# Optimization experiments

Hardware: AMD Instinct MI355X
Metric: run time of the kernel (lower is better)

The kernel has to match this reference:

```python
import jax, jax.numpy as jnp
import numpy as np


def _conv3x3(x, w, b):
    # NCHW conv, stride 1, pad 1
    y = jax.lax.conv_general_dilated(x, w, (1, 1), ((1, 1), (1, 1)),
                                     dimension_numbers=('NCHW', 'OIHW', 'NCHW'))
    return y + b[None, :, None, None]


def _deform_conv3x3(x, offset, w):
    # Deformable conv v1: 3x3, stride 1, pad 1, 1 deformable group, no bias.
    # offset: [B, 18, H, W] laid out as (dy_k, dx_k) for k = 0..8 (row-major taps).
    B, C, H, W = x.shape
    K = 9
    off = offset.reshape(B, K, 2, H, W)
    ky, kx = jnp.meshgrid(jnp.arange(3), jnp.arange(3), indexing='ij')
    ky = (ky.reshape(K) - 1).astype(x.dtype)  # kernel tap y-offset, pad=1
    kx = (kx.reshape(K) - 1).astype(x.dtype)
    hh = jnp.arange(H, dtype=x.dtype)
    ww = jnp.arange(W, dtype=x.dtype)
    # sampling locations [B, K, H, W]
    sy = hh[None, None, :, None] + ky[None, :, None, None] + off[:, :, 0]
    sx = ww[None, None, None, :] + kx[None, :, None, None] + off[:, :, 1]
    y0 = jnp.floor(sy)
    x0 = jnp.floor(sx)
    ly = sy - y0  # fractional parts
    lx = sx - x0
    x_flat = x.reshape(B, C, H * W)

    def gather(yi, xi, wgt):
        # zero-padding semantics: corners outside the image contribute 0
        valid = (yi >= 0) & (yi < H) & (xi >= 0) & (xi < W)
        idx = (jnp.clip(yi, 0, H - 1).astype(jnp.int32) * W
               + jnp.clip(xi, 0, W - 1).astype(jnp.int32)).reshape(B, 1, K * H * W)
        v = jnp.take_along_axis(x_flat, idx, axis=2).reshape(B, C, K, H, W)
        return v * (wgt * valid.astype(x.dtype))[:, None]

    sampled = (gather(y0,     x0,     (1 - ly) * (1 - lx))
             + gather(y0,     x0 + 1, (1 - ly) * lx)
             + gather(y0 + 1, x0,     ly * (1 - lx))
             + gather(y0 + 1, x0 + 1, ly * lx))  # [B, C, K, H, W]
    return jnp.einsum('bckhw,ock->bohw', sampled, w.reshape(w.shape[0], C, K))


def setup_inputs() -> dict:
    key = jax.random.key(0)
    ks = jax.random.split(key, 8)
    C, O = 256, 256
    return {
        'kernel': jax.random.normal(ks[0], (16, C, 16, 16), jnp.float32),
        'search': jax.random.normal(ks[1], (16, C, 32, 32), jnp.float32),
        'Toffset_w': jax.random.normal(ks[2], (18, C, 3, 3), jnp.float32) * 0.02,
        'Toffset_b': jnp.zeros((18,), jnp.float32),
        'Tdeform_w': jax.random.normal(ks[3], (O, C, 3, 3), jnp.float32) * 0.02,
        'Soffset_w': jax.random.normal(ks[4], (18, C, 3, 3), jnp.float32) * 0.02,
        'Soffset_b': jnp.zeros((18,), jnp.float32),
        'Sdeform_w': jax.random.normal(ks[5], (O, C, 3, 3), jnp.float32) * 0.02,
    }


def reference(kernel, search, Toffset_w, Toffset_b, Tdeform_w,
              Soffset_w, Soffset_b, Sdeform_w):
    kernel_offset = _conv3x3(kernel, Toffset_w, Toffset_b)
    kernel_out = _deform_conv3x3(kernel, kernel_offset, Tdeform_w)
    search_offset = _conv3x3(search, Soffset_w, Soffset_b)
    search_out = _deform_conv3x3(search, search_offset, Sdeform_w)
    return (kernel_out, search_out, kernel_offset, search_offset)
```

## Files before the change

kernel.cpp:

```cpp
#include <hip/hip_runtime.h>

#define CIN   256
#define OC    256
#define K_TOT 2304
#define CCH   32
#define NCHK  8
#define KCH   288
#define SSTR  296

#define N_DW  (OC * K_TOT)
#define N_OW  (32 * K_TOT)
#define N_CVT (2 * N_DW + 2 * N_OW)
#define CVT_BLOCKS (N_CVT / 4 / 256)

typedef short  bf16x8 __attribute__((ext_vector_type(8)));
typedef float  f32x4  __attribute__((ext_vector_type(4)));
typedef unsigned short ushort_t;

__device__ __forceinline__ ushort_t f2bf(float f) {
    unsigned u = __builtin_bit_cast(unsigned, f);
    u += 0x7fffu + ((u >> 16) & 1u);
    return (ushort_t)(u >> 16);
}
__device__ __forceinline__ float bf2f(short s) {
    return __builtin_bit_cast(float, ((unsigned)(unsigned short)s) << 16);
}

__global__ __launch_bounds__(256) void prep_k(
    const float* __restrict__ tdw, const float* __restrict__ sdw,
    const float* __restrict__ tow, const float* __restrict__ sow,
    const float* __restrict__ kin, const float* __restrict__ sin_,
    ushort_t* __restrict__ wk_d, ushort_t* __restrict__ ws_d,
    ushort_t* __restrict__ wk_o, ushort_t* __restrict__ ws_o,
    ushort_t* __restrict__ xt_k, ushort_t* __restrict__ xt_s)
{
    __shared__ ushort_t tile[64][264];

    if (blockIdx.x < CVT_BLOCKS) {
        const int i = (blockIdx.x * 256 + threadIdx.x) * 4;
        const float* src; ushort_t* dst; int j; bool offw = false;
        if (i < N_DW)                    { src = tdw; dst = wk_d; j = i; }
        else if (i < 2 * N_DW)           { src = sdw; dst = ws_d; j = i - N_DW; }
        else if (i < 2 * N_DW + N_OW)    { src = tow; dst = wk_o; j = i - 2 * N_DW; offw = true; }
        else                             { src = sow; dst = ws_o; j = i - 2 * N_DW - N_OW; offw = true; }
        const int oc = j / K_TOT;
        const int k  = j - oc * K_TOT;
        const int cc = k / KCH;
        const int r  = k - cc * KCH;
        const int tap = r >> 5;
        const int cl  = r & 31;
        ushort4 o4 = {0, 0, 0, 0};
        if (!offw || oc < 18) {
            const float* sp = &src[((size_t)oc * CIN + cc * 32 + cl) * 9 + tap];
            o4.x = f2bf(sp[0]); o4.y = f2bf(sp[9]); o4.z = f2bf(sp[18]); o4.w = f2bf(sp[27]);
        }
        *(ushort4*)&dst[j] = o4;
        return;
    }

    const int bx2 = blockIdx.x - CVT_BLOCKS;
    int H, W, b, px0; const float* x; ushort_t* xt;
    if (bx2 < 64) {
        H = 16; W = 16; x = kin; xt = xt_k;
        b = bx2 >> 2; px0 = (bx2 & 3) * 64;
    } else {
        int t2 = bx2 - 64;
        H = 32; W = 32; x = sin_; xt = xt_s;
        b = t2 >> 4; px0 = (t2 & 15) * 64;
    }
    const int HW = H * W;
    const int t = threadIdx.x, lane = t & 63, wv = t >> 6;
    const float* xb = x + (size_t)b * CIN * HW;

    for (int it = 0; it < 16; ++it) {
        const int ch = wv * 64 + it * 4 + (lane >> 4);
        const int pq = (lane & 15) * 4;
        float4 v = *(const float4*)&xb[(size_t)ch * HW + px0 + pq];
        tile[pq + 0][ch] = f2bf(v.x);
        tile[pq + 1][ch] = f2bf(v.y);
        tile[pq + 2][ch] = f2bf(v.z);
        tile[pq + 3][ch] = f2bf(v.w);
    }
    __syncthreads();
    for (int it = 0; it < 8; ++it) {
        const int px = it * 8 + wv * 2 + (lane >> 5);
        const int cg = (lane & 31) * 8;
        bf16x8 v = *(const bf16x8*)&tile[px][cg];
        *(bf16x8*)&xt[((size_t)b * HW + px0 + px) * 256 + cg] = v;
    }
}

__global__ __launch_bounds__(256, 2) void conv_gemm_k(
    const ushort_t* __restrict__ xt_k, const ushort_t* __restrict__ kwgt,
    const float* __restrict__ kbias, float* __restrict__ kout,
    const ushort_t* __restrict__ xt_s, const ushort_t* __restrict__ swgt,
    const float* __restrict__ sbias, float* __restrict__ sout)
{
    __shared__ float sred[2][64][4];

    int H, W, b, px0;
    const ushort_t* xt; const ushort_t* wgt; const float* bias; float* out;
    if (blockIdx.x < 256) {
        H = 16; W = 16; xt = xt_k; wgt = kwgt; bias = kbias; out = kout;
        b = blockIdx.x >> 4; px0 = (blockIdx.x & 15) * 16;
    } else {
        int t2 = blockIdx.x - 256;
        H = 32; W = 32; xt = xt_s; wgt = swgt; bias = sbias; out = sout;
        b = t2 >> 6; px0 = (t2 & 63) * 16;
    }
    const int HW = H * W;
    const int t = threadIdx.x, lane = t & 63, wv = t >> 6;
    const int l15 = lane & 15;
    const int cg8 = (lane >> 4) * 8;
    const int nt = wv & 1;
    const int kh = wv >> 1;

    const int px = px0 + l15;
    const int h  = px / W;
    const int wc = px - h * W;
    const ushort_t* xtb = xt + (size_t)b * HW * 256;

    int  aoff[9];
    bool aok [9];
#pragma unroll
    for (int ks = 0; ks < 9; ++ks) {
        const int y  = h + ks / 3 - 1;
        const int xx = wc + ks % 3 - 1;
        aok [ks] = ((unsigned)y < (unsigned)H) && ((unsigned)xx < (unsigned)W);
        aoff[ks] = aok[ks] ? ((y * W + xx) * 256 + cg8) : 0;
    }
    const ushort_t* wrow = wgt + (size_t)(nt * 16 + l15) * K_TOT + cg8;

    f32x4 acc = {};
    for (int cc = kh * 4; cc < kh * 4 + 4; ++cc) {
#pragma unroll
        for (int ks = 0; ks < 9; ++ks) {
            bf16x8 a = {};
            if (aok[ks]) a = *(const bf16x8*)&xtb[aoff[ks] + cc * 32];
            bf16x8 bb = *(const bf16x8*)&wrow[(size_t)cc * KCH + ks * 32];
            acc = __builtin_amdgcn_mfma_f32_16x16x32_bf16(a, bb, acc, 0, 0, 0);
        }
    }

    if (kh == 1) *(float4*)&sred[nt][lane][0] = *(float4*)&acc;
    __syncthreads();
    if (kh == 0) {
        const float4 o = *(const float4*)&sred[nt][lane][0];
        const int oc = nt * 16 + l15;
        if (oc < 18) {
            const float bs = bias[oc];
            const int prow = (lane >> 4) * 4;
            float4 r = { acc.x + o.x + bs, acc.y + o.y + bs,
                         acc.z + o.z + bs, acc.w + o.w + bs };
            *(float4*)(out + ((size_t)b * 18 + oc) * HW + px0 + prow) = r;
        }
    }
}

__device__ __forceinline__ void dcn_load4(
    bf16x8* c, const ushort_t* __restrict__ xtb, int4 id, int cb)
{
    c[0] = *(const bf16x8*)&xtb[(size_t)id.x * 256 + cb];
    c[1] = *(const bf16x8*)&xtb[(size_t)id.y * 256 + cb];
    c[2] = *(const bf16x8*)&xtb[(size_t)id.z * 256 + cb];
    c[3] = *(const bf16x8*)&xtb[(size_t)id.w * 256 + cb];
}
__device__ __forceinline__ void dcn_proc(
    ushort_t (*sw)[SSTR], int px, int tap, int cg, const bf16x8* c, float4 wt)
{
    bf16x8 r;
#pragma unroll
    for (int j = 0; j < 8; ++j) {
        const float v = wt.x * bf2f(c[0][j]) + wt.y * bf2f(c[1][j])
                      + wt.z * bf2f(c[2][j]) + wt.w * bf2f(c[3][j]);
        r[j] = (short)f2bf(v);
    }
    *(bf16x8*)&sw[px][tap * 32 + cg * 8] = r;
}
__device__ __forceinline__ void ldb2(
    bf16x8 (*B)[2], const ushort_t* __restrict__ w0,
    const ushort_t* __restrict__ w1, size_t kg0, int ks0)
{
    B[0][0] = *(const bf16x8*)&w0[kg0 + (size_t)ks0 * 32];
    B[0][1] = *(const bf16x8*)&w1[kg0 + (size_t)ks0 * 32];
    B[1][0] = *(const bf16x8*)&w0[kg0 + (size_t)(ks0 + 1) * 32];
    B[1][1] = *(const bf16x8*)&w1[kg0 + (size_t)(ks0 + 1) * 32];
}
__device__ __forceinline__ void mm2(
    f32x4 (*acc)[2], bf16x8 (*B)[2], ushort_t (*sw)[SSTR],
    int l15, int cg8, int ks0, int n)
{
#pragma unroll
    for (int i = 0; i < n; ++i) {
        bf16x8 a0 = *(const bf16x8*)&sw[l15     ][(ks0 + i) * 32 + cg8];
        bf16x8 a1 = *(const bf16x8*)&sw[16 + l15][(ks0 + i) * 32 + cg8];
        acc[0][0] = __builtin_amdgcn_mfma_f32_16x16x32_bf16(a0, B[i][0], acc[0][0], 0, 0, 0);
        acc[1][0] = __builtin_amdgcn_mfma_f32_16x16x32_bf16(a1, B[i][0], acc[1][0], 0, 0, 0);
        acc[0][1] = __builtin_amdgcn_mfma_f32_16x16x32_bf16(a0, B[i][1], acc[0][1], 0, 0, 0);
        acc[1][1] = __builtin_amdgcn_mfma_f32_16x16x32_bf16(a1, B[i][1], acc[1][1], 0, 0, 0);
    }
}

__global__ __launch_bounds__(512, 4) void deform_gemm_k(
    const ushort_t* __restrict__ xt_k, const float* __restrict__ koffs,
    const ushort_t* __restrict__ kwgt, float* __restrict__ kout,
    const ushort_t* __restrict__ xt_s, const float* __restrict__ soffs,
    const ushort_t* __restrict__ swgt_, float* __restrict__ sout)
{
    __shared__ __align__(16) ushort_t smp[2][32][SSTR];
    __shared__ __align__(16) int      sidx[32][9][4];
    __shared__ __align__(16) float    swt [32][9][4];

    int H, W, b, px0;
    const ushort_t* xt; const float* offs; const ushort_t* wgt; float* out;
    if (blockIdx.x < 128) {
        H = 16; W = 16; xt = xt_k; offs = koffs; wgt = kwgt; out = kout;
        b = blockIdx.x >> 3; px0 = (blockIdx.x & 7) * 32;
    } else {
        int t2 = blockIdx.x - 128;
        H = 32; W = 32; xt = xt_s; offs = soffs; wgt = swgt_; out = sout;
        b = t2 >> 5; px0 = (t2 & 31) * 32;
    }
    const int HW = H * W;
    const int t = threadIdx.x, lane = t & 63, wv = t >> 6;

    if (t < 288) {
        const int p = t / 9, k = t - 9 * p;
        const int pix = px0 + p;
        const int h  = pix / W;
        const int wc = pix - h * W;
        const float* ob = offs + (size_t)b * 18 * HW;
        const float dy = ob[(2 * k    ) * HW + pix];
        const float dx = ob[(2 * k + 1) * HW + pix];
        const float sy = (float)(h  + k / 3 - 1) + dy;
        const float sx = (float)(wc + k % 3 - 1) + dx;
        const float y0f = floorf(sy), x0f = floorf(sx);
        const float ly = sy - y0f, lx = sx - x0f;
        const int y0 = (int)y0f, x0 = (int)x0f;
#pragma unroll
        for (int j = 0; j < 4; ++j) {
            const int yy = y0 + (j >> 1);
            const int xx = x0 + (j & 1);
            const bool ok = ((unsigned)yy < (unsigned)H) && ((unsigned)xx < (unsigned)W);
            sidx[p][k][j] = min(max(yy, 0), H - 1) * W + min(max(xx, 0), W - 1);
            const float wj = ((j >> 1) ? ly : 1.f - ly) * ((j & 1) ? lx : 1.f - lx);
            swt[p][k][j] = ok ? wj : 0.f;
        }
    }
    __syncthreads();

    const ushort_t* xtb = xt + (size_t)b * HW * 256;
    const int l15 = lane & 15;
    const int cg8 = (lane >> 4) * 8;
    const int ocb = wv * 32;

    int upx[3], utap[3], ucg[3];
#pragma unroll
    for (int u = 0; u < 3; ++u) {
        const int s = t + u * 512;
        if (s < 1152) {
            utap[u] = s >> 7;
            const int r = s & 127;
            upx[u] = r >> 2; ucg[u] = r & 3;
        }
    }
    const bool live2 = (t < 128);

    const ushort_t* wrow0 = wgt + (size_t)(ocb      + l15) * K_TOT + cg8;
    const ushort_t* wrow1 = wgt + (size_t)(ocb + 16 + l15) * K_TOT + cg8;

    f32x4 acc[2][2] = {};

    for (int cc = 0; cc < NCHK; ++cc) {
        ushort_t (*sw)[SSTR] = smp[cc & 1];
        const int cb = cc * 32;
        const size_t kg0 = (size_t)cc * KCH;

        bf16x8 c0[4], c1[4], c2[4];
        const int4   id0 = *(const int4*)  sidx[upx[0]][utap[0]];
        const float4 wt0 = *(const float4*)swt [upx[0]][utap[0]];
        const int4   id1 = *(const int4*)  sidx[upx[1]][utap[1]];
        const float4 wt1 = *(const float4*)swt [upx[1]][utap[1]];
        dcn_load4(c0, xtb, id0, cb + ucg[0] * 8);
        dcn_load4(c1, xtb, id1, cb + ucg[1] * 8);
        int4 id2 = {}; float4 wt2 = {};
        if (live2) {
            id2 = *(const int4*)  sidx[upx[2]][utap[2]];
            wt2 = *(const float4*)swt [upx[2]][utap[2]];
            dcn_load4(c2, xtb, id2, cb + ucg[2] * 8);
        }
        dcn_proc(sw, upx[0], utap[0], ucg[0], c0, wt0);
        bf16x8 bX[2][2], bY[2][2];
        ldb2(bX, wrow0, wrow1, kg0, 0);
        dcn_proc(sw, upx[1], utap[1], ucg[1], c1, wt1);
        if (live2) dcn_proc(sw, upx[2], utap[2], ucg[2], c2, wt2);
        __syncthreads();

        ldb2(bY, wrow0, wrow1, kg0, 2);  mm2(acc, bX, sw, l15, cg8, 0, 2);
        ldb2(bX, wrow0, wrow1, kg0, 4);  mm2(acc, bY, sw, l15, cg8, 2, 2);
        ldb2(bY, wrow0, wrow1, kg0, 6);  mm2(acc, bX, sw, l15, cg8, 4, 2);
        bX[0][0] = *(const bf16x8*)&wrow0[kg0 + 8 * 32];
        bX[0][1] = *(const bf16x8*)&wrow1[kg0 + 8 * 32];
        mm2(acc, bY, sw, l15, cg8, 6, 2);
        mm2(acc, bX, sw, l15, cg8, 8, 1);
    }

    const int prow = (lane >> 4) * 4;
#pragma unroll
    for (int mt = 0; mt < 2; ++mt) {
#pragma unroll
        for (int nt = 0; nt < 2; ++nt) {
            const int oc = ocb + nt * 16 + l15;
            float* op = out + ((size_t)b * OC + oc) * HW + px0 + mt * 16 + prow;
            *(float4*)op = *(float4*)&acc[mt][nt];
        }
    }
}

extern "C" void kernel_launch(void* const* d_in, const int* in_sizes, int n_in,
                              void* d_out, int out_size, void* d_ws, size_t ws_size,
                              hipStream_t stream) {
    const float* kin = (const float*)d_in[0];
    const float* sin_ = (const float*)d_in[1];
    const float* tow = (const float*)d_in[2];
    const float* tob = (const float*)d_in[3];
    const float* tdw = (const float*)d_in[4];
    const float* sow = (const float*)d_in[5];
    const float* sob = (const float*)d_in[6];
    const float* sdw = (const float*)d_in[7];

    float* out = (float*)d_out;
    float* out_k  = out;
    float* out_s  = out_k + (size_t)16 * 256 * 16 * 16;
    float* out_ko = out_s + (size_t)16 * 256 * 32 * 32;
    float* out_so = out_ko + (size_t)16 * 18 * 16 * 16;

    ushort_t* wk_d = (ushort_t*)d_ws;
    ushort_t* ws_d = wk_d + N_DW;
    ushort_t* wk_o = ws_d + N_DW;
    ushort_t* ws_o = wk_o + N_OW;
    ushort_t* xt_k = ws_o + N_OW;
    ushort_t* xt_s = xt_k + (size_t)16 * 256 * 256;

    prep_k<<<dim3(CVT_BLOCKS + 320), 256, 0, stream>>>(
        tdw, sdw, tow, sow, kin, sin_,
        wk_d, ws_d, wk_o, ws_o, xt_k, xt_s);

    conv_gemm_k<<<dim3(1280), 256, 0, stream>>>(
        xt_k, wk_o, tob, out_ko, xt_s, ws_o, sob, out_so);

    deform_gemm_k<<<dim3(640), 512, 0, stream>>>(
        xt_k, out_ko, wk_d, out_k, xt_s, out_so, ws_d, out_s);
}
```

Baseline: 246.4 us.

## Prefetch next channel chunk's bilinear gathers across the MFMA phase

The deformable-conv main loop now issues the global gathers for chunk cc+1 right after writing chunk cc's interpolated samples to LDS, so their latency overlaps the MFMA work instead of stalling at the start of each iteration. Per-unit element offsets, weights and LDS store offsets are precomputed once before the loop. The __syncthreads is replaced by an LDS-only waitcnt plus raw s_barrier with sched barriers, so outstanding global loads need not drain, and the MFMA section runs at raised wave priority. This keeps about 12 more bf16x8 values live per thread, which raises register pressure and may lower occupancy.

```diff
diff --git a/kernel.cpp b/kernel.cpp
--- a/kernel.cpp
+++ b/kernel.cpp
@@ -157,16 +157,16 @@
     }
 }
 
-__device__ __forceinline__ void dcn_load4(
-    bf16x8* c, const ushort_t* __restrict__ xtb, int4 id, int cb)
-{
-    c[0] = *(const bf16x8*)&xtb[(size_t)id.x * 256 + cb];
-    c[1] = *(const bf16x8*)&xtb[(size_t)id.y * 256 + cb];
-    c[2] = *(const bf16x8*)&xtb[(size_t)id.z * 256 + cb];
-    c[3] = *(const bf16x8*)&xtb[(size_t)id.w * 256 + cb];
-}
-__device__ __forceinline__ void dcn_proc(
-    ushort_t (*sw)[SSTR], int px, int tap, int cg, const bf16x8* c, float4 wt)
+__device__ __forceinline__ void dcn_load4o(
+    bf16x8* c, const ushort_t* __restrict__ xtb, int4 eo, int cb)
+{
+    c[0] = *(const bf16x8*)&xtb[eo.x + cb];
+    c[1] = *(const bf16x8*)&xtb[eo.y + cb];
+    c[2] = *(const bf16x8*)&xtb[eo.z + cb];
+    c[3] = *(const bf16x8*)&xtb[eo.w + cb];
+}
+__device__ __forceinline__ void dcn_proc2(
+    ushort_t* swb, int so, const bf16x8* c, float4 wt)
 {
     bf16x8 r;
 #pragma unroll
@@ -175,7 +175,23 @@
                       + wt.z * bf2f(c[2][j]) + wt.w * bf2f(c[3][j]);
         r[j] = (short)f2bf(v);
     }
-    *(bf16x8*)&sw[px][tap * 32 + cg * 8] = r;
+    *(bf16x8*)&swb[so] = r;
+}
+__device__ __forceinline__ void unit_params(
+    int s, const int (*sidx)[9][4], const float (*swt)[9][4],
+    int4& eo, float4& wt, int& so)
+{
+    const int tap = s >> 7;
+    const int r   = s & 127;
+    const int px  = r >> 2;
+    const int cg  = r & 3;
+    const int4 id = *(const int4*)sidx[px][tap];
+    eo.x = id.x * 256 + cg * 8;
+    eo.y = id.y * 256 + cg * 8;
+    eo.z = id.z * 256 + cg * 8;
+    eo.w = id.w * 256 + cg * 8;
+    wt = *(const float4*)swt[px][tap];
+    so = px * SSTR + tap * 32 + cg * 8;
 }
 __device__ __forceinline__ void ldb2(
     bf16x8 (*B)[2], const ushort_t* __restrict__ w0,
@@ -253,49 +269,49 @@
     const int l15 = lane & 15;
     const int cg8 = (lane >> 4) * 8;
     const int ocb = wv * 32;
-
-    int upx[3], utap[3], ucg[3];
-#pragma unroll
-    for (int u = 0; u < 3; ++u) {
-        const int s = t + u * 512;
-        if (s < 1152) {
-            utap[u] = s >> 7;
-            const int r = s & 127;
-            upx[u] = r >> 2; ucg[u] = r & 3;
-        }
-    }
     const bool live2 = (t < 128);
+
+    int4 eoff0, eoff1, eoff2 = {};
+    float4 uwt0, uwt1, uwt2 = {};
+    int swo0, swo1, swo2 = 0;
+    unit_params(t,        sidx, swt, eoff0, uwt0, swo0);
+    unit_params(t + 512,  sidx, swt, eoff1, uwt1, swo1);
+    if (live2) unit_params(t + 1024, sidx, swt, eoff2, uwt2, swo2);
 
     const ushort_t* wrow0 = wgt + (size_t)(ocb      + l15) * K_TOT + cg8;
     const ushort_t* wrow1 = wgt + (size_t)(ocb + 16 + l15) * K_TOT + cg8;
 
     f32x4 acc[2][2] = {};
+    bf16x8 c0[4], c1[4], c2[4];
+
+    dcn_load4o(c0, xtb, eoff0, 0);
+    dcn_load4o(c1, xtb, eoff1, 0);
+    if (live2) dcn_load4o(c2, xtb, eoff2, 0);
 
     for (int cc = 0; cc < NCHK; ++cc) {
         ushort_t (*sw)[SSTR] = smp[cc & 1];
-        const int cb = cc * 32;
+        ushort_t* swb = &sw[0][0];
         const size_t kg0 = (size_t)cc * KCH;
 
-        bf16x8 c0[4], c1[4], c2[4];
-        const int4   id0 = *(const int4*)  sidx[upx[0]][utap[0]];
-        const float4 wt0 = *(const float4*)swt [upx[0]][utap[0]];
-        const int4   id1 = *(const int4*)  sidx[upx[1]][utap[1]];
-        const float4 wt1 = *(const float4*)swt [upx[1]][utap[1]];
-        dcn_load4(c0, xtb, id0, cb + ucg[0] * 8);
-        dcn_load4(c1, xtb, id1, cb + ucg[1] * 8);
-        int4 id2 = {}; float4 wt2 = {};
-        if (live2) {
-            id2 = *(const int4*)  sidx[upx[2]][utap[2]];
-            wt2 = *(const float4*)swt [upx[2]][utap[2]];
-            dcn_load4(c2, xtb, id2, cb + ucg[2] * 8);
-        }
-        dcn_proc(sw, upx[0], utap[0], ucg[0], c0, wt0);
         bf16x8 bX[2][2], bY[2][2];
+        dcn_proc2(swb, swo0, c0, uwt0);
         ldb2(bX, wrow0, wrow1, kg0, 0);
-        dcn_proc(sw, upx[1], utap[1], ucg[1], c1, wt1);
-        if (live2) dcn_proc(sw, upx[2], utap[2], ucg[2], c2, wt2);
-        __syncthreads();
-
+        dcn_proc2(swb, swo1, c1, uwt1);
+        if (live2) dcn_proc2(swb, swo2, c2, uwt2);
+
+        if (cc < NCHK - 1) {
+            const int cb = (cc + 1) * 32;
+            dcn_load4o(c0, xtb, eoff0, cb);
+            dcn_load4o(c1, xtb, eoff1, cb);
+            if (live2) dcn_load4o(c2, xtb, eoff2, cb);
+        }
+
+        asm volatile("s_waitcnt lgkmcnt(0)" ::: "memory");
+        __builtin_amdgcn_sched_barrier(0);
+        __builtin_amdgcn_s_barrier();
+        __builtin_amdgcn_sched_barrier(0);
+
+        __builtin_amdgcn_s_setprio(1);
         ldb2(bY, wrow0, wrow1, kg0, 2);  mm2(acc, bX, sw, l15, cg8, 0, 2);
         ldb2(bX, wrow0, wrow1, kg0, 4);  mm2(acc, bY, sw, l15, cg8, 2, 2);
         ldb2(bY, wrow0, wrow1, kg0, 6);  mm2(acc, bX, sw, l15, cg8, 4, 2);
@@ -303,6 +319,7 @@
         bX[0][1] = *(const bf16x8*)&wrow1[kg0 + 8 * 32];
         mm2(acc, bY, sw, l15, cg8, 6, 2);
         mm2(acc, bX, sw, l15, cg8, 8, 1);
+        __builtin_amdgcn_s_setprio(0);
     }
 
     const int prow = (lane >> 4) * 4;
```

Result: slower. 275.0 us (+11.6%).

## Enlarge pixel tiles to 64 in offset conv and deformable GEMM kernels

Applied to the files above, without the earlier changes.

The offset conv kernel now computes 64 pixels by 32 output channels per block, with the input-channel reduction split four ways across waves, so each weight fragment is reused over four M-tiles. The deformable GEMM kernel processes 64 pixels per block with a single-buffered sample tile, reorganised sample-build indexing, explicit barriers and raised MFMA priority. Both grids shrink to 320 blocks. This cuts weight reloads and per-block overhead, in exchange for more registers, a single LDS buffer that needs two barriers per chunk, and fewer blocks to fill the GPU.

```diff
diff --git a/kernel.cpp b/kernel.cpp
--- a/kernel.cpp
+++ b/kernel.cpp
@@ -7,6 +7,8 @@
 #define NCHK  8
 #define KCH   288
 #define SSTR  296
+#define DM    64
+#define DUNITS (DM * 9 * 4)
 
 #define N_DW  (OC * K_TOT)
 #define N_OW  (32 * K_TOT)
@@ -96,63 +98,82 @@
     const ushort_t* __restrict__ xt_s, const ushort_t* __restrict__ swgt,
     const float* __restrict__ sbias, float* __restrict__ sout)
 {
-    __shared__ float sred[2][64][4];
-
-    int H, W, b, px0;
+    __shared__ float sred[3][4][2][64][4];
+
+    int H, W, sh, b, px0;
     const ushort_t* xt; const ushort_t* wgt; const float* bias; float* out;
-    if (blockIdx.x < 256) {
-        H = 16; W = 16; xt = xt_k; wgt = kwgt; bias = kbias; out = kout;
-        b = blockIdx.x >> 4; px0 = (blockIdx.x & 15) * 16;
+    if (blockIdx.x < 64) {
+        H = 16; W = 16; sh = 4; xt = xt_k; wgt = kwgt; bias = kbias; out = kout;
+        b = blockIdx.x >> 2; px0 = (blockIdx.x & 3) * 64;
     } else {
-        int t2 = blockIdx.x - 256;
-        H = 32; W = 32; xt = xt_s; wgt = swgt; bias = sbias; out = sout;
-        b = t2 >> 6; px0 = (t2 & 63) * 16;
+        int t2 = blockIdx.x - 64;
+        H = 32; W = 32; sh = 5; xt = xt_s; wgt = swgt; bias = sbias; out = sout;
+        b = t2 >> 4; px0 = (t2 & 15) * 64;
     }
     const int HW = H * W;
-    const int t = threadIdx.x, lane = t & 63, wv = t >> 6;
+    const int t = threadIdx.x, lane = t & 63, kh = t >> 6;
     const int l15 = lane & 15;
     const int cg8 = (lane >> 4) * 8;
-    const int nt = wv & 1;
-    const int kh = wv >> 1;
-
-    const int px = px0 + l15;
-    const int h  = px / W;
-    const int wc = px - h * W;
     const ushort_t* xtb = xt + (size_t)b * HW * 256;
 
-    int  aoff[9];
-    bool aok [9];
-#pragma unroll
-    for (int ks = 0; ks < 9; ++ks) {
-        const int y  = h + ks / 3 - 1;
-        const int xx = wc + ks % 3 - 1;
-        aok [ks] = ((unsigned)y < (unsigned)H) && ((unsigned)xx < (unsigned)W);
-        aoff[ks] = aok[ks] ? ((y * W + xx) * 256 + cg8) : 0;
-    }
-    const ushort_t* wrow = wgt + (size_t)(nt * 16 + l15) * K_TOT + cg8;
-
-    f32x4 acc = {};
-    for (int cc = kh * 4; cc < kh * 4 + 4; ++cc) {
+    int h[4], wc[4];
+#pragma unroll
+    for (int mt = 0; mt < 4; ++mt) {
+        const int px = px0 + mt * 16 + l15;
+        h[mt]  = px >> sh;
+        wc[mt] = px & (W - 1);
+    }
+    const ushort_t* wrow0 = wgt + (size_t)(l15)      * K_TOT + cg8;
+    const ushort_t* wrow1 = wgt + (size_t)(16 + l15) * K_TOT + cg8;
+
+    f32x4 acc[4][2] = {};
+    for (int cc = kh * 2; cc < kh * 2 + 2; ++cc) {
+        const int cb = cc * 32 + cg8;
 #pragma unroll
         for (int ks = 0; ks < 9; ++ks) {
-            bf16x8 a = {};
-            if (aok[ks]) a = *(const bf16x8*)&xtb[aoff[ks] + cc * 32];
-            bf16x8 bb = *(const bf16x8*)&wrow[(size_t)cc * KCH + ks * 32];
-            acc = __builtin_amdgcn_mfma_f32_16x16x32_bf16(a, bb, acc, 0, 0, 0);
-        }
-    }
-
-    if (kh == 1) *(float4*)&sred[nt][lane][0] = *(float4*)&acc;
+            const bf16x8 b0 = *(const bf16x8*)&wrow0[(size_t)cc * KCH + ks * 32];
+            const bf16x8 b1 = *(const bf16x8*)&wrow1[(size_t)cc * KCH + ks * 32];
+            const int dy = ks / 3 - 1, dx = ks % 3 - 1;
+#pragma unroll
+            for (int mt = 0; mt < 4; ++mt) {
+                const int y  = h[mt] + dy;
+                const int xx = wc[mt] + dx;
+                const bool ok = ((unsigned)y < (unsigned)H) && ((unsigned)xx < (unsigned)W);
+                bf16x8 a = {};
+                if (ok) a = *(const bf16x8*)&xtb[(size_t)(((y << sh) + xx) * 256 + cb)];
+                acc[mt][0] = __builtin_amdgcn_mfma_f32_16x16x32_bf16(a, b0, acc[mt][0], 0, 0, 0);
+                acc[mt][1] = __builtin_amdgcn_mfma_f32_16x16x32_bf16(a, b1, acc[mt][1], 0, 0, 0);
+            }
+        }
+    }
+
+    if (kh > 0) {
+#pragma unroll
+        for (int mt = 0; mt < 4; ++mt)
+#pragma unroll
+            for (int nt = 0; nt < 2; ++nt)
+                *(float4*)&sred[kh - 1][mt][nt][lane][0] = *(float4*)&acc[mt][nt];
+    }
     __syncthreads();
     if (kh == 0) {
-        const float4 o = *(const float4*)&sred[nt][lane][0];
-        const int oc = nt * 16 + l15;
-        if (oc < 18) {
-            const float bs = bias[oc];
-            const int prow = (lane >> 4) * 4;
-            float4 r = { acc.x + o.x + bs, acc.y + o.y + bs,
-                         acc.z + o.z + bs, acc.w + o.w + bs };
-            *(float4*)(out + ((size_t)b * 18 + oc) * HW + px0 + prow) = r;
+        const int prow = (lane >> 4) * 4;
+#pragma unroll
+        for (int nt = 0; nt < 2; ++nt) {
+            const int oc = nt * 16 + l15;
+            if (oc < 18) {
+                const float bs = bias[oc];
+#pragma unroll
+                for (int mt = 0; mt < 4; ++mt) {
+                    float4 r = *(float4*)&acc[mt][nt];
+#pragma unroll
+                    for (int q = 0; q < 3; ++q) {
+                        const float4 o = *(const float4*)&sred[q][mt][nt][lane][0];
+                        r.x += o.x; r.y += o.y; r.z += o.z; r.w += o.w;
+                    }
+                    r.x += bs; r.y += bs; r.z += bs; r.w += bs;
+                    *(float4*)(out + ((size_t)b * 18 + oc) * HW + px0 + mt * 16 + prow) = r;
+                }
+            }
         }
     }
 }
@@ -165,8 +186,8 @@
     c[2] = *(const bf16x8*)&xtb[(size_t)id.z * 256 + cb];
     c[3] = *(const bf16x8*)&xtb[(size_t)id.w * 256 + cb];
 }
-__device__ __forceinline__ void dcn_proc(
-    ushort_t (*sw)[SSTR], int px, int tap, int cg, const bf16x8* c, float4 wt)
+__device__ __forceinline__ void dcn_proc2(
+    ushort_t* swb, int so, const bf16x8* c, float4 wt)
 {
     bf16x8 r;
 #pragma unroll
@@ -175,30 +196,7 @@
                       + wt.z * bf2f(c[2][j]) + wt.w * bf2f(c[3][j]);
         r[j] = (short)f2bf(v);
     }
-    *(bf16x8*)&sw[px][tap * 32 + cg * 8] = r;
-}
-__device__ __forceinline__ void ldb2(
-    bf16x8 (*B)[2], const ushort_t* __restrict__ w0,
-    const ushort_t* __restrict__ w1, size_t kg0, int ks0)
-{
-    B[0][0] = *(const bf16x8*)&w0[kg0 + (size_t)ks0 * 32];
-    B[0][1] = *(const bf16x8*)&w1[kg0 + (size_t)ks0 * 32];
-    B[1][0] = *(const bf16x8*)&w0[kg0 + (size_t)(ks0 + 1) * 32];
-    B[1][1] = *(const bf16x8*)&w1[kg0 + (size_t)(ks0 + 1) * 32];
-}
-__device__ __forceinline__ void mm2(
-    f32x4 (*acc)[2], bf16x8 (*B)[2], ushort_t (*sw)[SSTR],
-    int l15, int cg8, int ks0, int n)
-{
-#pragma unroll
-    for (int i = 0; i < n; ++i) {
-        bf16x8 a0 = *(const bf16x8*)&sw[l15     ][(ks0 + i) * 32 + cg8];
-        bf16x8 a1 = *(const bf16x8*)&sw[16 + l15][(ks0 + i) * 32 + cg8];
-        acc[0][0] = __builtin_amdgcn_mfma_f32_16x16x32_bf16(a0, B[i][0], acc[0][0], 0, 0, 0);
-        acc[1][0] = __builtin_amdgcn_mfma_f32_16x16x32_bf16(a1, B[i][0], acc[1][0], 0, 0, 0);
-        acc[0][1] = __builtin_amdgcn_mfma_f32_16x16x32_bf16(a0, B[i][1], acc[0][1], 0, 0, 0);
-        acc[1][1] = __builtin_amdgcn_mfma_f32_16x16x32_bf16(a1, B[i][1], acc[1][1], 0, 0, 0);
-    }
+    *(bf16x8*)&swb[so] = r;
 }
 
 __global__ __launch_bounds__(512, 4) void deform_gemm_k(
@@ -207,44 +205,48 @@
     const ushort_t* __restrict__ xt_s, const float* __restrict__ soffs,
     const ushort_t* __restrict__ swgt_, float* __restrict__ sout)
 {
-    __shared__ __align__(16) ushort_t smp[2][32][SSTR];
-    __shared__ __align__(16) int      sidx[32][9][4];
-    __shared__ __align__(16) float    swt [32][9][4];
+    __shared__ __align__(16) ushort_t smp[DM][SSTR];
+    __shared__ __align__(16) int      sidx[DM][9][4];
+    __shared__ __align__(16) float    swt [DM][9][4];
 
     int H, W, b, px0;
     const ushort_t* xt; const float* offs; const ushort_t* wgt; float* out;
-    if (blockIdx.x < 128) {
+    if (blockIdx.x < 64) {
         H = 16; W = 16; xt = xt_k; offs = koffs; wgt = kwgt; out = kout;
-        b = blockIdx.x >> 3; px0 = (blockIdx.x & 7) * 32;
+        b = blockIdx.x >> 2; px0 = (blockIdx.x & 3) * 64;
     } else {
-        int t2 = blockIdx.x - 128;
+        int t2 = blockIdx.x - 64;
         H = 32; W = 32; xt = xt_s; offs = soffs; wgt = swgt_; out = sout;
-        b = t2 >> 5; px0 = (t2 & 31) * 32;
+        b = t2 >> 4; px0 = (t2 & 15) * 64;
     }
     const int HW = H * W;
     const int t = threadIdx.x, lane = t & 63, wv = t >> 6;
 
-    if (t < 288) {
-        const int p = t / 9, k = t - 9 * p;
-        const int pix = px0 + p;
-        const int h  = pix / W;
-        const int wc = pix - h * W;
-        const float* ob = offs + (size_t)b * 18 * HW;
-        const float dy = ob[(2 * k    ) * HW + pix];
-        const float dx = ob[(2 * k + 1) * HW + pix];
-        const float sy = (float)(h  + k / 3 - 1) + dy;
-        const float sx = (float)(wc + k % 3 - 1) + dx;
-        const float y0f = floorf(sy), x0f = floorf(sx);
-        const float ly = sy - y0f, lx = sx - x0f;
-        const int y0 = (int)y0f, x0 = (int)x0f;
-#pragma unroll
-        for (int j = 0; j < 4; ++j) {
-            const int yy = y0 + (j >> 1);
-            const int xx = x0 + (j & 1);
-            const bool ok = ((unsigned)yy < (unsigned)H) && ((unsigned)xx < (unsigned)W);
-            sidx[p][k][j] = min(max(yy, 0), H - 1) * W + min(max(xx, 0), W - 1);
-            const float wj = ((j >> 1) ? ly : 1.f - ly) * ((j & 1) ? lx : 1.f - lx);
-            swt[p][k][j] = ok ? wj : 0.f;
+#pragma unroll
+    for (int u = 0; u < 2; ++u) {
+        const int s = t + u * 512;
+        if (s < DM * 9) {
+            const int p = s / 9, k = s - 9 * p;
+            const int pix = px0 + p;
+            const int h  = pix / W;
+            const int wc = pix - h * W;
+            const float* ob = offs + (size_t)b * 18 * HW;
+            const float dy = ob[(2 * k    ) * HW + pix];
+            const float dx = ob[(2 * k + 1) * HW + pix];
+            const float sy = (float)(h  + k / 3 - 1) + dy;
+            const float sx = (float)(wc + k % 3 - 1) + dx;
+            const float y0f = floorf(sy), x0f = floorf(sx);
+            const float ly = sy - y0f, lx = sx - x0f;
+            const int y0 = (int)y0f, x0 = (int)x0f;
+#pragma unroll
+            for (int j = 0; j < 4; ++j) {
+                const int yy = y0 + (j >> 1);
+                const int xx = x0 + (j & 1);
+                const bool ok = ((unsigned)yy < (unsigned)H) && ((unsigned)xx < (unsigned)W);
+                sidx[p][k][j] = min(max(yy, 0), H - 1) * W + min(max(xx, 0), W - 1);
+                const float wj = ((j >> 1) ? ly : 1.f - ly) * ((j & 1) ? lx : 1.f - lx);
+                swt[p][k][j] = ok ? wj : 0.f;
+            }
         }
     }
     __syncthreads();
@@ -253,61 +255,77 @@
     const int l15 = lane & 15;
     const int cg8 = (lane >> 4) * 8;
     const int ocb = wv * 32;
-
-    int upx[3], utap[3], ucg[3];
-#pragma unroll
-    for (int u = 0; u < 3; ++u) {
-        const int s = t + u * 512;
-        if (s < 1152) {
-            utap[u] = s >> 7;
-            const int r = s & 127;
-            upx[u] = r >> 2; ucg[u] = r & 3;
-        }
-    }
-    const bool live2 = (t < 128);
+    const bool live4 = (t < 256);
+
+    const int g0  = t >> 2;
+    const int cgE = (t & 3) * 8;
+    int uso[5];
+#pragma unroll
+    for (int q = 0; q < 5; ++q) {
+        const int g  = g0 + q * 128;
+        const int px = g / 9, tap = g - 9 * px;
+        uso[q] = px * SSTR + tap * 32 + (t & 3) * 8;
+    }
 
     const ushort_t* wrow0 = wgt + (size_t)(ocb      + l15) * K_TOT + cg8;
     const ushort_t* wrow1 = wgt + (size_t)(ocb + 16 + l15) * K_TOT + cg8;
-
-    f32x4 acc[2][2] = {};
+    ushort_t* smpb = &smp[0][0];
+    const int4*   sidxF = (const int4*)  &sidx[0][0][0];
+    const float4* swtF  = (const float4*)&swt [0][0][0];
+
+    f32x4 acc[4][2] = {};
 
     for (int cc = 0; cc < NCHK; ++cc) {
-        ushort_t (*sw)[SSTR] = smp[cc & 1];
-        const int cb = cc * 32;
+        const int cb = cc * 32 + cgE;
         const size_t kg0 = (size_t)cc * KCH;
 
-        bf16x8 c0[4], c1[4], c2[4];
-        const int4   id0 = *(const int4*)  sidx[upx[0]][utap[0]];
-        const float4 wt0 = *(const float4*)swt [upx[0]][utap[0]];
-        const int4   id1 = *(const int4*)  sidx[upx[1]][utap[1]];
-        const float4 wt1 = *(const float4*)swt [upx[1]][utap[1]];
-        dcn_load4(c0, xtb, id0, cb + ucg[0] * 8);
-        dcn_load4(c1, xtb, id1, cb + ucg[1] * 8);
-        int4 id2 = {}; float4 wt2 = {};
-        if (live2) {
-            id2 = *(const int4*)  sidx[upx[2]][utap[2]];
-            wt2 = *(const float4*)swt [upx[2]][utap[2]];
-            dcn_load4(c2, xtb, id2, cb + ucg[2] * 8);
-        }
-        dcn_proc(sw, upx[0], utap[0], ucg[0], c0, wt0);
-        bf16x8 bX[2][2], bY[2][2];
-        ldb2(bX, wrow0, wrow1, kg0, 0);
-        dcn_proc(sw, upx[1], utap[1], ucg[1], c1, wt1);
-        if (live2) dcn_proc(sw, upx[2], utap[2], ucg[2], c2, wt2);
-        __syncthreads();
-
-        ldb2(bY, wrow0, wrow1, kg0, 2);  mm2(acc, bX, sw, l15, cg8, 0, 2);
-        ldb2(bX, wrow0, wrow1, kg0, 4);  mm2(acc, bY, sw, l15, cg8, 2, 2);
-        ldb2(bY, wrow0, wrow1, kg0, 6);  mm2(acc, bX, sw, l15, cg8, 4, 2);
-        bX[0][0] = *(const bf16x8*)&wrow0[kg0 + 8 * 32];
-        bX[0][1] = *(const bf16x8*)&wrow1[kg0 + 8 * 32];
-        mm2(acc, bY, sw, l15, cg8, 6, 2);
-        mm2(acc, bX, sw, l15, cg8, 8, 1);
+#pragma unroll
+        for (int q = 0; q < 5; ++q) {
+            if (q < 4 || live4) {
+                const int  g  = g0 + q * 128;
+                const int4   id = sidxF[g];
+                const float4 wt = swtF[g];
+                bf16x8 c[4];
+                dcn_load4(c, xtb, id, cb);
+                dcn_proc2(smpb, uso[q], c, wt);
+            }
+        }
+
+        const bf16x8 pb0 = *(const bf16x8*)&wrow0[kg0];
+        const bf16x8 pb1 = *(const bf16x8*)&wrow1[kg0];
+
+        asm volatile("s_waitcnt lgkmcnt(0)" ::: "memory");
+        __builtin_amdgcn_sched_barrier(0);
+        __builtin_amdgcn_s_barrier();
+        __builtin_amdgcn_sched_barrier(0);
+
+        __builtin_amdgcn_s_setprio(1);
+#pragma unroll
+        for (int ks = 0; ks < 9; ++ks) {
+            const bf16x8 b0 = (ks == 0) ? pb0 : *(const bf16x8*)&wrow0[kg0 + (size_t)ks * 32];
+            const bf16x8 b1 = (ks == 0) ? pb1 : *(const bf16x8*)&wrow1[kg0 + (size_t)ks * 32];
+            bf16x8 a[4];
+#pragma unroll
+            for (int mt = 0; mt < 4; ++mt)
+                a[mt] = *(const bf16x8*)&smp[mt * 16 + l15][ks * 32 + cg8];
+#pragma unroll
+            for (int mt = 0; mt < 4; ++mt) {
+                acc[mt][0] = __builtin_amdgcn_mfma_f32_16x16x32_bf16(a[mt], b0, acc[mt][0], 0, 0, 0);
+                acc[mt][1] = __builtin_amdgcn_mfma_f32_16x16x32_bf16(a[mt], b1, acc[mt][1], 0, 0, 0);
+            }
+        }
+        __builtin_amdgcn_s_setprio(0);
+
+        if (cc < NCHK - 1) {
+            __builtin_amdgcn_sched_barrier(0);
+            __builtin_amdgcn_s_barrier();
+            __builtin_amdgcn_sched_barrier(0);
+        }
     }
 
     const int prow = (lane >> 4) * 4;
 #pragma unroll
-    for (int mt = 0; mt < 2; ++mt) {
+    for (int mt = 0; mt < 4; ++mt) {
 #pragma unroll
         for (int nt = 0; nt < 2; ++nt) {
             const int oc = ocb + nt * 16 + l15;
@@ -346,9 +364,9 @@
         tdw, sdw, tow, sow, kin, sin_,
         wk_d, ws_d, wk_o, ws_o, xt_k, xt_s);
 
-    conv_gemm_k<<<dim3(1280), 256, 0, stream>>>(
+    conv_gemm_k<<<dim3(320), 256, 0, stream>>>(
         xt_k, wk_o, tob, out_ko, xt_s, ws_o, sob, out_so);
 
-    deform_gemm_k<<<dim3(640), 512, 0, stream>>>(
+    deform_gemm_k<<<dim3(320), 512, 0, stream>>>(
         xt_k, out_ko, wk_d, out_k, xt_s, out_so, ws_d, out_s);
 }
```

New measurement: 207.7 us. 15.7% less time.
